# Optimization experiments

Measured on AMD Instinct MI355X. Metric: run time of the kernel, lower is better.

Reference implementation:

```python
import jax, jax.numpy as jnp
import numpy as np

S = 3072      # total tokens across all images
DIM = 1280    # hidden_size
H = 16        # num_heads
HD = DIM // H # head_dim = 80
NSEG = 6      # number of images (cu_seqlens has NSEG+1 entries)


def _rotate_half(x):
    x1, x2 = jnp.split(x, 2, axis=-1)
    return jnp.concatenate([-x2, x1], axis=-1)


def setup_inputs() -> dict:
    key = jax.random.key(0)
    ks = jax.random.split(key, 12)
    hidden_states = jax.random.normal(ks[0], (S, DIM), jnp.float32)
    # realistic vision rotary embedding: half-dim inv_freq, repeated to head_dim
    inv_freq = 1.0 / (10000.0 ** (jnp.arange(0, HD // 2, dtype=jnp.float32) / (HD // 2)))
    freqs = jnp.arange(S, dtype=jnp.float32)[:, None] * inv_freq[None, :]  # [S, HD/2]
    emb = jnp.concatenate([freqs, freqs], axis=-1)  # [S, HD]
    cos = jnp.cos(emb)
    sin = jnp.sin(emb)
    sc = 0.02
    wq = jax.random.normal(ks[1], (DIM, DIM), jnp.float32) * sc
    bq = jax.random.normal(ks[2], (DIM,), jnp.float32) * sc
    wk = jax.random.normal(ks[3], (DIM, DIM), jnp.float32) * sc
    bk = jax.random.normal(ks[4], (DIM,), jnp.float32) * sc
    wv = jax.random.normal(ks[5], (DIM, DIM), jnp.float32) * sc
    bv = jax.random.normal(ks[6], (DIM,), jnp.float32) * sc
    wo = jax.random.normal(ks[7], (DIM, DIM), jnp.float32) * sc
    bo = jax.random.normal(ks[8], (DIM,), jnp.float32) * sc
    cu_seqlens = (jnp.arange(NSEG + 1, dtype=jnp.int32) * (S // NSEG))  # [0,512,...,3072]
    return dict(hidden_states=hidden_states, cos=cos, sin=sin,
                wq=wq, bq=bq, wk=wk, bk=bk, wv=wv, bv=bv, wo=wo, bo=bo,
                cu_seqlens=cu_seqlens)


def reference(hidden_states, cos, sin, wq, bq, wk, bk, wv, bv, wo, bo, cu_seqlens):
    seq_length = hidden_states.shape[0]
    scaling = HD ** (-0.5)
    # QKV projections (torch Linear: x @ W.T + b)
    q = (hidden_states @ wq.T + bq).reshape(seq_length, H, HD)
    k = (hidden_states @ wk.T + bk).reshape(seq_length, H, HD)
    v = (hidden_states @ wv.T + bv).reshape(seq_length, H, HD)
    # apply_rotary_pos_emb_vision: cos/sin [S, HD] broadcast over head axis
    c = cos[:, None, :]
    s = sin[:, None, :]
    q = q * c + _rotate_half(q) * s
    k = k * c + _rotate_half(k) * s
    # block-diagonal (per-image) attention via segment mask
    seg = jnp.searchsorted(cu_seqlens[1:], jnp.arange(seq_length), side='right')
    mask = seg[:, None] == seg[None, :]  # [S, S] bool
    scores = jnp.einsum('shd,thd->hst', q, k) * scaling  # [H, S, S]
    scores = jnp.where(mask[None, :, :], scores, jnp.finfo(scores.dtype).min)
    attn = jax.nn.softmax(scores, axis=-1)
    out = jnp.einsum('hst,thd->shd', attn, v).reshape(seq_length, DIM)
    return out @ wo.T + bo
```

## Files before the change

### kernel.cpp

```cpp
#include <hip/hip_runtime.h>
#include <hip/hip_bf16.h>
#include <hip/hip_fp16.h>
#include <cstdint>
#include <cstddef>

typedef _Float16 f16;
typedef f16 f16x2 __attribute__((ext_vector_type(2)));
typedef f16 f16x4 __attribute__((ext_vector_type(4)));
typedef f16 f16x8 __attribute__((ext_vector_type(8)));
typedef float f32x4 __attribute__((ext_vector_type(4)));

#define S_LEN 3072
#define DIM 1280
#define NH 16
#define HD 80
#define SEG 512

#define MFMA16F(a, b, c) __builtin_amdgcn_mfma_f32_16x16x32_f16((a), (b), (c), 0, 0, 0)

__device__ __forceinline__ void gl2lds16(const void* g, void* l) {
    __builtin_amdgcn_global_load_lds(
        (const __attribute__((address_space(1))) unsigned int*)g,
        (__attribute__((address_space(3))) unsigned int*)l, 16, 0, 0);
}

__device__ __forceinline__ unsigned int pack2(float a, float b) {
    f16x2 t = {(f16)a, (f16)b};
    union { f16x2 v; unsigned int u; } c;
    c.v = t;
    return c.u;
}

__global__ __launch_bounds__(256) void cvt_kernel(
    const float* __restrict__ hs,
    const float* __restrict__ wq, const float* __restrict__ wk,
    const float* __restrict__ wv, const float* __restrict__ wo,
    f16* __restrict__ hs16,
    f16* __restrict__ wq16, f16* __restrict__ wk16,
    f16* __restrict__ wv16, f16* __restrict__ wo16)
{
    const int m = blockIdx.y;
    const float* src; f16* dst; int n4;
    if (m == 0)      { src = hs; dst = hs16; n4 = S_LEN * DIM / 4; }
    else if (m == 1) { src = wq; dst = wq16; n4 = DIM * DIM / 4; }
    else if (m == 2) { src = wk; dst = wk16; n4 = DIM * DIM / 4; }
    else if (m == 3) { src = wv; dst = wv16; n4 = DIM * DIM / 4; }
    else             { src = wo; dst = wo16; n4 = DIM * DIM / 4; }
    int idx = blockIdx.x * 256 + threadIdx.x;
    if (idx >= n4) return;
    f32x4 v = *(const f32x4*)(src + (size_t)idx * 4);
    f16x4 o;
#pragma unroll
    for (int e = 0; e < 4; ++e) o[e] = (f16)v[e];
    *(f16x4*)(dst + (size_t)idx * 4) = o;
}

__global__ __launch_bounds__(256) void gemm_f16_kernel(
    const f16* __restrict__ A,
    const f16* __restrict__ W0, const f16* __restrict__ W1, const f16* __restrict__ W2,
    const float* __restrict__ b0, const float* __restrict__ b1, const float* __restrict__ b2,
    f16* __restrict__ O0, f16* __restrict__ O1, f16* __restrict__ vT)
{
    const int f = blockIdx.x;
    const int xcd = f & 7;
    const int idx = f >> 3;
    const int mt = xcd * 3 + idx % 3;
    const int yz = idx / 3;
    const int nt = yz % 10;
    const int mode = yz / 10;

    const f16* W = (mode == 1) ? W1 : (mode == 2) ? W2 : W0;
    const float* bias = (mode == 1) ? b1 : (mode == 2) ? b2 : b0;

    __shared__ __align__(16) f16 As[128 * 32];
    __shared__ __align__(16) f16 Bs[128 * 32];

    const int tid = threadIdx.x;
    const int lane = tid & 63;
    const int lane15 = tid & 15;
    const int quad = lane >> 4;
    const int w = tid >> 6;
    const int wm = (w >> 1) * 64;
    const int wn = (w & 1) * 64;
    const int m0 = mt * 128;
    const int n0 = nt * 128;

    const int srow = w * 32 + (lane >> 2);
    const int scol = (lane & 3) * 8;
    const f16* gA0 = A + (size_t)(m0 + srow) * DIM + scol;
    const f16* gA1 = A + (size_t)(m0 + srow + 16) * DIM + scol;
    const f16* gB0 = W + (size_t)(n0 + srow) * DIM + scol;
    const f16* gB1 = W + (size_t)(n0 + srow + 16) * DIM + scol;
    f16* lA0 = As + (w * 32) * 32;
    f16* lA1 = As + (w * 32 + 16) * 32;
    f16* lB0 = Bs + (w * 32) * 32;
    f16* lB1 = Bs + (w * 32 + 16) * 32;

    f32x4 acc[4][4];
#pragma unroll
    for (int i = 0; i < 4; ++i)
#pragma unroll
        for (int j = 0; j < 4; ++j)
            acc[i][j] = (f32x4){0.f, 0.f, 0.f, 0.f};

    for (int kt = 0; kt < DIM / 32; ++kt) {
        __syncthreads();
        gl2lds16(gA0 + kt * 32, lA0);
        gl2lds16(gA1 + kt * 32, lA1);
        gl2lds16(gB0 + kt * 32, lB0);
        gl2lds16(gB1 + kt * 32, lB1);
        __syncthreads();

        f16x8 fa[4], fb[4];
#pragma unroll
        for (int i = 0; i < 4; ++i)
            fa[i] = *(const f16x8*)(As + (wm + i * 16 + lane15) * 32 + quad * 8);
#pragma unroll
        for (int j = 0; j < 4; ++j)
            fb[j] = *(const f16x8*)(Bs + (wn + j * 16 + lane15) * 32 + quad * 8);
#pragma unroll
        for (int i = 0; i < 4; ++i)
#pragma unroll
            for (int j = 0; j < 4; ++j)
                acc[i][j] = MFMA16F(fa[i], fb[j], acc[i][j]);
    }

    float bvv[4];
#pragma unroll
    for (int j = 0; j < 4; ++j)
        bvv[j] = bias[n0 + wn + j * 16 + lane15];

    if (mode == 2) {
#pragma unroll
        for (int i = 0; i < 4; ++i)
#pragma unroll
            for (int j = 0; j < 4; ++j) {
                f16x4 ov;
#pragma unroll
                for (int r = 0; r < 4; ++r) ov[r] = (f16)(acc[i][j][r] + bvv[j]);
                int row = m0 + wm + i * 16 + quad * 4;
                int col = n0 + wn + j * 16 + lane15;
                *(f16x4*)(vT + (size_t)col * S_LEN + row) = ov;
            }
    } else {
        f16* O = (mode == 0) ? O0 : O1;
#pragma unroll
        for (int i = 0; i < 4; ++i)
#pragma unroll
            for (int j = 0; j < 4; ++j)
#pragma unroll
                for (int r = 0; r < 4; ++r) {
                    int row = m0 + wm + i * 16 + quad * 4 + r;
                    int col = n0 + wn + j * 16 + lane15;
                    O[(size_t)row * DIM + col] = (f16)(acc[i][j][r] + bvv[j]);
                }
    }
}

__global__ __launch_bounds__(256) void gemm_out_kernel(
    const f16* __restrict__ A, const f16* __restrict__ W,
    const float* __restrict__ bias, float* __restrict__ OF)
{
    const int f = blockIdx.x;
    const int xcd = f & 7;
    const int idx = f >> 3;
    const int xt = xcd * 6 + idx % 6;
    const int yt = idx / 6;

    __shared__ __align__(16) f16 As[64 * 32];
    __shared__ __align__(16) f16 Bs[128 * 32];

    const int tid = threadIdx.x;
    const int lane = tid & 63;
    const int lane15 = tid & 15;
    const int quad = lane >> 4;
    const int w = tid >> 6;
    const int wn = w * 32;
    const int m0 = xt * 64;
    const int n0 = yt * 128;

    const int srA = w * 16 + (lane >> 2);
    const int srB = w * 32 + (lane >> 2);
    const int scol = (lane & 3) * 8;
    const f16* gA0 = A + (size_t)(m0 + srA) * DIM + scol;
    const f16* gB0 = W + (size_t)(n0 + srB) * DIM + scol;
    const f16* gB1 = W + (size_t)(n0 + srB + 16) * DIM + scol;
    f16* lA0 = As + (w * 16) * 32;
    f16* lB0 = Bs + (w * 32) * 32;
    f16* lB1 = Bs + (w * 32 + 16) * 32;

    f32x4 acc[4][2];
#pragma unroll
    for (int i = 0; i < 4; ++i)
#pragma unroll
        for (int j = 0; j < 2; ++j)
            acc[i][j] = (f32x4){0.f, 0.f, 0.f, 0.f};

    for (int kt = 0; kt < DIM / 32; ++kt) {
        __syncthreads();
        gl2lds16(gA0 + kt * 32, lA0);
        gl2lds16(gB0 + kt * 32, lB0);
        gl2lds16(gB1 + kt * 32, lB1);
        __syncthreads();

        f16x8 fa[4], fb[2];
#pragma unroll
        for (int i = 0; i < 4; ++i)
            fa[i] = *(const f16x8*)(As + (i * 16 + lane15) * 32 + quad * 8);
#pragma unroll
        for (int j = 0; j < 2; ++j)
            fb[j] = *(const f16x8*)(Bs + (wn + j * 16 + lane15) * 32 + quad * 8);
#pragma unroll
        for (int i = 0; i < 4; ++i)
#pragma unroll
            for (int j = 0; j < 2; ++j)
                acc[i][j] = MFMA16F(fa[i], fb[j], acc[i][j]);
    }

    float bvv[2];
#pragma unroll
    for (int j = 0; j < 2; ++j)
        bvv[j] = bias[n0 + wn + j * 16 + lane15];

#pragma unroll
    for (int i = 0; i < 4; ++i)
#pragma unroll
        for (int j = 0; j < 2; ++j)
#pragma unroll
            for (int r = 0; r < 4; ++r) {
                int row = m0 + i * 16 + quad * 4 + r;
                int col = n0 + wn + j * 16 + lane15;
                OF[(size_t)row * DIM + col] = acc[i][j][r] + bvv[j];
            }
}

__global__ __launch_bounds__(256) void rope_kernel(
    f16* __restrict__ qb, f16* __restrict__ kb,
    const float* __restrict__ cosb, const float* __restrict__ sinb)
{
    int idx = blockIdx.x * 256 + threadIdx.x;
    int c = idx % 5;
    int t = idx / 5;
    int h = t & 15; t >>= 4;
    int s = t % S_LEN;
    int which = t / S_LEN;
    f16* buf = which ? kb : qb;
    float scale = which ? 1.0f : 0.11180339887498948f;
    int j = c * 8;
    f32x4 ca = *(const f32x4*)(cosb + s * HD + j);
    f32x4 cb = *(const f32x4*)(cosb + s * HD + j + 4);
    f32x4 sna = *(const f32x4*)(sinb + s * HD + j);
    f32x4 snb = *(const f32x4*)(sinb + s * HD + j + 4);
    size_t base = (size_t)s * DIM + h * HD + j;
    f16x8 x1 = *(f16x8*)(buf + base);
    f16x8 x2 = *(f16x8*)(buf + base + 40);
    f16x8 o1, o2;
#pragma unroll
    for (int e = 0; e < 8; ++e) {
        float ce = (e < 4) ? ca[e] : cb[e - 4];
        float se = (e < 4) ? sna[e] : snb[e - 4];
        float a = (float)x1[e], b = (float)x2[e];
        o1[e] = (f16)((a * ce - b * se) * scale);
        o2[e] = (f16)((b * ce + a * se) * scale);
    }
    *(f16x8*)(buf + base) = o1;
    *(f16x8*)(buf + base + 40) = o2;
}

__global__ __launch_bounds__(256) void attn_kernel(
    const f16* __restrict__ q, const f16* __restrict__ k,
    const f16* __restrict__ vT, f16* __restrict__ o)
{
    const int h = blockIdx.x;
    const int g = blockIdx.y;
    const int qc = blockIdx.z;
    const int tid = threadIdx.x;
    const int lane15 = tid & 15;
    const int quad = (tid & 63) >> 4;
    const int w = tid >> 6;
    const int qbase = g * SEG + qc * 64;
    const int qrow = qbase + w * 16 + lane15;

    __shared__ __align__(16) f16 Ks[128 * 88];
    __shared__ __align__(16) f16 Vt[80 * 128];

    f16x8 zf;
#pragma unroll
    for (int e = 0; e < 8; ++e) zf[e] = (f16)0.0f;

    f16x8 fq[3];
#pragma unroll
    for (int kc = 0; kc < 3; ++kc) {
        if (kc == 2 && quad >= 2) fq[kc] = zf;
        else fq[kc] = *(const f16x8*)(q + (size_t)qrow * DIM + h * HD + kc * 32 + quad * 8);
    }

    float m_run = -1e30f, l_run = 0.f;
    f32x4 Oa[5];
#pragma unroll
    for (int dt = 0; dt < 5; ++dt) Oa[dt] = (f32x4){0.f, 0.f, 0.f, 0.f};

    for (int kt = 0; kt < 4; ++kt) {
        __syncthreads();
        const int kb = g * SEG + kt * 128;
#pragma unroll
        for (int c = tid; c < 1280; c += 256) {
            int r = c / 10;
            int c8 = (c - r * 10) * 8;
            *(f16x8*)(Ks + r * 88 + c8) =
                *(const f16x8*)(k + (size_t)(kb + r) * DIM + h * HD + c8);
        }
#pragma unroll
        for (int c = tid; c < 1280; c += 256) {
            int d = c >> 4;
            int sc = c & 15;
            *(f16x8*)(Vt + d * 128 + (sc ^ (d & 7)) * 8) =
                *(const f16x8*)(vT + (size_t)(h * HD + d) * S_LEN + kb + sc * 8);
        }
        __syncthreads();

        f32x4 sa[8];
#pragma unroll
        for (int nt = 0; nt < 8; ++nt) sa[nt] = (f32x4){0.f, 0.f, 0.f, 0.f};
#pragma unroll
        for (int kc = 0; kc < 3; ++kc) {
#pragma unroll
            for (int nt = 0; nt < 8; ++nt) {
                f16x8 fk;
                if (kc == 2 && quad >= 2) fk = zf;
                else fk = *(const f16x8*)(Ks + (nt * 16 + lane15) * 88 + kc * 32 + quad * 8);
                sa[nt] = MFMA16F(fk, fq[kc], sa[nt]);
            }
        }

        float mt = -1e30f;
#pragma unroll
        for (int nt = 0; nt < 8; ++nt)
#pragma unroll
            for (int r = 0; r < 4; ++r) mt = fmaxf(mt, sa[nt][r]);
        mt = fmaxf(mt, __shfl_xor(mt, 16, 64));
        mt = fmaxf(mt, __shfl_xor(mt, 32, 64));

        float mn = fmaxf(m_run, mt);
        float alpha = __expf(m_run - mn);
        m_run = mn;
        float lt = 0.f;
        unsigned int pp[8][2];
#pragma unroll
        for (int nt = 0; nt < 8; ++nt) {
            float p0 = __expf(sa[nt][0] - mn);
            float p1 = __expf(sa[nt][1] - mn);
            float p2 = __expf(sa[nt][2] - mn);
            float p3 = __expf(sa[nt][3] - mn);
            lt += (p0 + p1) + (p2 + p3);
            pp[nt][0] = pack2(p0, p1);
            pp[nt][1] = pack2(p2, p3);
        }
        lt += __shfl_xor(lt, 16, 64);
        lt += __shfl_xor(lt, 32, 64);
        l_run = l_run * alpha + lt;

#pragma unroll
        for (int dt = 0; dt < 5; ++dt)
#pragma unroll
            for (int r = 0; r < 4; ++r) Oa[dt][r] *= alpha;

        const int srcA = ((quad & 1) * 2) * 16 + lane15;
        const int srcB = srcA + 16;
        const bool hi = quad >= 2;
#pragma unroll
        for (int kc2 = 0; kc2 < 4; ++kc2) {
            unsigned int e0 = __shfl((int)pp[2 * kc2][0], srcA, 64);
            unsigned int e1 = __shfl((int)pp[2 * kc2][1], srcA, 64);
            unsigned int e2 = __shfl((int)pp[2 * kc2][0], srcB, 64);
            unsigned int e3 = __shfl((int)pp[2 * kc2][1], srcB, 64);
            unsigned int o0 = __shfl((int)pp[2 * kc2 + 1][0], srcA, 64);
            unsigned int o1 = __shfl((int)pp[2 * kc2 + 1][1], srcA, 64);
            unsigned int o2 = __shfl((int)pp[2 * kc2 + 1][0], srcB, 64);
            unsigned int o3 = __shfl((int)pp[2 * kc2 + 1][1], srcB, 64);
            union { unsigned int u[4]; f16x8 v; } fp;
            fp.u[0] = hi ? o0 : e0;
            fp.u[1] = hi ? o1 : e1;
            fp.u[2] = hi ? o2 : e2;
            fp.u[3] = hi ? o3 : e3;
#pragma unroll
            for (int dt = 0; dt < 5; ++dt) {
                int drow = dt * 16 + lane15;
                int slot = (kc2 * 4 + quad) ^ (drow & 7);
                f16x8 fv = *(const f16x8*)(Vt + drow * 128 + slot * 8);
                Oa[dt] = MFMA16F(fv, fp.v, Oa[dt]);
            }
        }
    }

    float inv = 1.0f / l_run;
#pragma unroll
    for (int dt = 0; dt < 5; ++dt) {
        f16x4 ov;
#pragma unroll
        for (int r = 0; r < 4; ++r) ov[r] = (f16)(Oa[dt][r] * inv);
        *(f16x4*)(o + (size_t)qrow * DIM + h * HD + dt * 16 + quad * 4) = ov;
    }
}

extern "C" void kernel_launch(void* const* d_in, const int* in_sizes, int n_in,
                              void* d_out, int out_size, void* d_ws, size_t ws_size,
                              hipStream_t stream)
{
    const float* hs   = (const float*)d_in[0];
    const float* cosb = (const float*)d_in[1];
    const float* sinb = (const float*)d_in[2];
    const float* wq   = (const float*)d_in[3];
    const float* bq   = (const float*)d_in[4];
    const float* wk   = (const float*)d_in[5];
    const float* bk   = (const float*)d_in[6];
    const float* wv   = (const float*)d_in[7];
    const float* bv   = (const float*)d_in[8];
    const float* wo   = (const float*)d_in[9];
    const float* bo   = (const float*)d_in[10];

    const size_t SD = (size_t)S_LEN * DIM;
    const size_t WW = (size_t)DIM * DIM;
    f16* hs16 = (f16*)d_ws;
    f16* wq16 = hs16 + SD;
    f16* wk16 = wq16 + WW;
    f16* wv16 = wk16 + WW;
    f16* wo16 = wv16 + WW;
    f16* q16  = wo16 + WW;
    f16* k16  = q16 + SD;
    f16* vT16 = k16 + SD;
    f16* ao16 = vT16 + SD;
    float* outb = (float*)d_out;

    cvt_kernel<<<dim3(S_LEN * DIM / 4 / 256, 5), 256, 0, stream>>>(
        hs, wq, wk, wv, wo, hs16, wq16, wk16, wv16, wo16);
    gemm_f16_kernel<<<720, 256, 0, stream>>>(
        hs16, wq16, wk16, wv16, bq, bk, bv, q16, k16, vT16);
    rope_kernel<<<1920, 256, 0, stream>>>(q16, k16, cosb, sinb);
    attn_kernel<<<dim3(NH, 6, 8), 256, 0, stream>>>(q16, k16, vT16, ao16);
    gemm_out_kernel<<<480, 256, 0, stream>>>(ao16, wo16, bo, outb);
}
```

Before: 217.9 us.

## Rewrite QKV GEMM with 256x256 tiles, double-buffered LDS and swizzled layout

Replaces the 128x128 QKV projection kernel with a 256x256-tile, 512-thread kernel that treats the wq/wk/wv f16 copies as one contiguous 3840-row weight matrix. It double-buffers the K=64 slabs in LDS, prefetching the next slab during compute, and uses an XOR-swizzled LDS layout to avoid bank conflicts. MFMA phases are interleaved with barriers and s_setprio. The larger tiles raise data reuse and cut launch count from 720 to 180 blocks, but this may leave CUs underfilled on a 256-CU part and needs 128KB of LDS per block. It also assumes the three weight buffers sit contiguously in the workspace, which they do.

```diff
diff --git a/kernel.cpp b/kernel.cpp
--- a/kernel.cpp
+++ b/kernel.cpp
@@ -55,105 +55,173 @@
     *(f16x4*)(dst + (size_t)idx * 4) = o;
 }
 
-__global__ __launch_bounds__(256) void gemm_f16_kernel(
-    const f16* __restrict__ A,
-    const f16* __restrict__ W0, const f16* __restrict__ W1, const f16* __restrict__ W2,
-    const float* __restrict__ b0, const float* __restrict__ b1, const float* __restrict__ b2,
-    f16* __restrict__ O0, f16* __restrict__ O1, f16* __restrict__ vT)
+__global__ __launch_bounds__(512, 2) void gemm_qkv256(
+    const f16* __restrict__ A, const f16* __restrict__ Wb,
+    const float* __restrict__ bq, const float* __restrict__ bk,
+    const float* __restrict__ bv,
+    f16* __restrict__ q16, f16* __restrict__ k16, f16* __restrict__ vT)
 {
-    const int f = blockIdx.x;
-    const int xcd = f & 7;
-    const int idx = f >> 3;
-    const int mt = xcd * 3 + idx % 3;
-    const int yz = idx / 3;
-    const int nt = yz % 10;
-    const int mode = yz / 10;
-
-    const f16* W = (mode == 1) ? W1 : (mode == 2) ? W2 : W0;
-    const float* bias = (mode == 1) ? b1 : (mode == 2) ? b2 : b0;
-
-    __shared__ __align__(16) f16 As[128 * 32];
-    __shared__ __align__(16) f16 Bs[128 * 32];
+    const int bid = blockIdx.x;
+    const int mt = bid / 15;
+    const int nt = bid % 15;
+    const int m0 = mt * 256;
+    const int n0 = nt * 256;
+
+    __shared__ __align__(16) f16 Abuf[2][256 * 64];
+    __shared__ __align__(16) f16 Bbuf[2][256 * 64];
 
     const int tid = threadIdx.x;
+    const int w = tid >> 6;
     const int lane = tid & 63;
-    const int lane15 = tid & 15;
+    const int lane15 = lane & 15;
     const int quad = lane >> 4;
-    const int w = tid >> 6;
-    const int wm = (w >> 1) * 64;
-    const int wn = (w & 1) * 64;
-    const int m0 = mt * 128;
-    const int n0 = nt * 128;
-
-    const int srow = w * 32 + (lane >> 2);
-    const int scol = (lane & 3) * 8;
-    const f16* gA0 = A + (size_t)(m0 + srow) * DIM + scol;
-    const f16* gA1 = A + (size_t)(m0 + srow + 16) * DIM + scol;
-    const f16* gB0 = W + (size_t)(n0 + srow) * DIM + scol;
-    const f16* gB1 = W + (size_t)(n0 + srow + 16) * DIM + scol;
-    f16* lA0 = As + (w * 32) * 32;
-    f16* lA1 = As + (w * 32 + 16) * 32;
-    f16* lB0 = Bs + (w * 32) * 32;
-    f16* lB1 = Bs + (w * 32 + 16) * 32;
-
-    f32x4 acc[4][4];
-#pragma unroll
-    for (int i = 0; i < 4; ++i)
+    const int wm = (w >> 2) * 128;
+    const int wn = (w & 3) * 64;
+
+    const int srow = lane >> 3;
+    const int schk = (lane & 7) ^ srow;
+    const f16* gA = A  + (size_t)(m0 + w * 32 + srow) * DIM + schk * 8;
+    const f16* gB = Wb + (size_t)(n0 + w * 32 + srow) * DIM + schk * 8;
+
+    const int x7 = lane15 & 7;
+    const int cc0 = (quad ^ x7) * 8;
+    const int cc1 = ((quad + 4) ^ x7) * 8;
+
+    f32x4 acc[8][4];
+#pragma unroll
+    for (int i = 0; i < 8; ++i)
 #pragma unroll
         for (int j = 0; j < 4; ++j)
             acc[i][j] = (f32x4){0.f, 0.f, 0.f, 0.f};
 
-    for (int kt = 0; kt < DIM / 32; ++kt) {
-        __syncthreads();
-        gl2lds16(gA0 + kt * 32, lA0);
-        gl2lds16(gA1 + kt * 32, lA1);
-        gl2lds16(gB0 + kt * 32, lB0);
-        gl2lds16(gB1 + kt * 32, lB1);
-        __syncthreads();
-
-        f16x8 fa[4], fb[4];
+#pragma unroll
+    for (int c = 0; c < 4; ++c)
+        gl2lds16(gA + (size_t)c * 8 * DIM, Abuf[0] + (w * 4 + c) * 512);
+#pragma unroll
+    for (int c = 0; c < 4; ++c)
+        gl2lds16(gB + (size_t)c * 8 * DIM, Bbuf[0] + (w * 4 + c) * 512);
+    asm volatile("s_waitcnt vmcnt(0)" ::: "memory");
+    __builtin_amdgcn_s_barrier();
+
+    for (int kt = 0; kt < 20; ++kt) {
+        const int s = kt & 1;
+        const f16* As = Abuf[s];
+        const f16* Bs = Bbuf[s];
+
+        if (kt < 19) {
+            const f16* gA1 = gA + (kt + 1) * 64;
+            const f16* gB1 = gB + (kt + 1) * 64;
+            f16* lA = Abuf[s ^ 1] + w * 4 * 512;
+            f16* lB = Bbuf[s ^ 1] + w * 4 * 512;
+#pragma unroll
+            for (int c = 0; c < 4; ++c) gl2lds16(gA1 + (size_t)c * 8 * DIM, lA + c * 512);
+#pragma unroll
+            for (int c = 0; c < 4; ++c) gl2lds16(gB1 + (size_t)c * 8 * DIM, lB + c * 512);
+        }
+        f16x8 a0[4][2], b01[2][2];
+#pragma unroll
+        for (int i = 0; i < 4; ++i) {
+            const f16* rp = As + (wm + i * 16 + lane15) * 64;
+            a0[i][0] = *(const f16x8*)(rp + cc0);
+            a0[i][1] = *(const f16x8*)(rp + cc1);
+        }
+#pragma unroll
+        for (int j = 0; j < 2; ++j) {
+            const f16* rp = Bs + (wn + j * 16 + lane15) * 64;
+            b01[j][0] = *(const f16x8*)(rp + cc0);
+            b01[j][1] = *(const f16x8*)(rp + cc1);
+        }
+        __builtin_amdgcn_s_setprio(1);
 #pragma unroll
         for (int i = 0; i < 4; ++i)
-            fa[i] = *(const f16x8*)(As + (wm + i * 16 + lane15) * 32 + quad * 8);
-#pragma unroll
-        for (int j = 0; j < 4; ++j)
-            fb[j] = *(const f16x8*)(Bs + (wn + j * 16 + lane15) * 32 + quad * 8);
+#pragma unroll
+            for (int j = 0; j < 2; ++j) {
+                acc[i][j] = MFMA16F(a0[i][0], b01[j][0], acc[i][j]);
+                acc[i][j] = MFMA16F(a0[i][1], b01[j][1], acc[i][j]);
+            }
+        __builtin_amdgcn_s_setprio(0);
+        __builtin_amdgcn_s_barrier();
+
+        f16x8 b23[2][2];
+#pragma unroll
+        for (int j = 0; j < 2; ++j) {
+            const f16* rp = Bs + (wn + (j + 2) * 16 + lane15) * 64;
+            b23[j][0] = *(const f16x8*)(rp + cc0);
+            b23[j][1] = *(const f16x8*)(rp + cc1);
+        }
+        __builtin_amdgcn_s_setprio(1);
 #pragma unroll
         for (int i = 0; i < 4; ++i)
 #pragma unroll
+            for (int j = 0; j < 2; ++j) {
+                acc[i][j + 2] = MFMA16F(a0[i][0], b23[j][0], acc[i][j + 2]);
+                acc[i][j + 2] = MFMA16F(a0[i][1], b23[j][1], acc[i][j + 2]);
+            }
+        __builtin_amdgcn_s_setprio(0);
+        __builtin_amdgcn_s_barrier();
+
+        f16x8 a1[4][2];
+#pragma unroll
+        for (int i = 0; i < 4; ++i) {
+            const f16* rp = As + (wm + (i + 4) * 16 + lane15) * 64;
+            a1[i][0] = *(const f16x8*)(rp + cc0);
+            a1[i][1] = *(const f16x8*)(rp + cc1);
+        }
+        __builtin_amdgcn_s_setprio(1);
+#pragma unroll
+        for (int i = 0; i < 4; ++i)
+#pragma unroll
+            for (int j = 0; j < 2; ++j) {
+                acc[i + 4][j + 2] = MFMA16F(a1[i][0], b23[j][0], acc[i + 4][j + 2]);
+                acc[i + 4][j + 2] = MFMA16F(a1[i][1], b23[j][1], acc[i + 4][j + 2]);
+            }
+        __builtin_amdgcn_s_setprio(0);
+        __builtin_amdgcn_s_barrier();
+
+        __builtin_amdgcn_s_setprio(1);
+#pragma unroll
+        for (int i = 0; i < 4; ++i)
+#pragma unroll
+            for (int j = 0; j < 2; ++j) {
+                acc[i + 4][j] = MFMA16F(a1[i][0], b01[j][0], acc[i + 4][j]);
+                acc[i + 4][j] = MFMA16F(a1[i][1], b01[j][1], acc[i + 4][j]);
+            }
+        __builtin_amdgcn_s_setprio(0);
+        asm volatile("s_waitcnt vmcnt(0)" ::: "memory");
+        __builtin_amdgcn_s_barrier();
+    }
+
+    const int sel = nt / 5;
+    const int nc0 = n0 - sel * 1280 + wn;
+    const float* bias = (sel == 0) ? bq : (sel == 1) ? bk : bv;
+    float bvv[4];
+#pragma unroll
+    for (int j = 0; j < 4; ++j) bvv[j] = bias[nc0 + j * 16 + lane15];
+
+    if (sel < 2) {
+        f16* O = sel ? k16 : q16;
+#pragma unroll
+        for (int i = 0; i < 8; ++i)
+#pragma unroll
             for (int j = 0; j < 4; ++j)
-                acc[i][j] = MFMA16F(fa[i], fb[j], acc[i][j]);
-    }
-
-    float bvv[4];
-#pragma unroll
-    for (int j = 0; j < 4; ++j)
-        bvv[j] = bias[n0 + wn + j * 16 + lane15];
-
-    if (mode == 2) {
-#pragma unroll
-        for (int i = 0; i < 4; ++i)
+#pragma unroll
+                for (int r = 0; r < 4; ++r) {
+                    int row = m0 + wm + i * 16 + quad * 4 + r;
+                    O[(size_t)row * DIM + nc0 + j * 16 + lane15] =
+                        (f16)(acc[i][j][r] + bvv[j]);
+                }
+    } else {
+#pragma unroll
+        for (int i = 0; i < 8; ++i)
 #pragma unroll
             for (int j = 0; j < 4; ++j) {
                 f16x4 ov;
 #pragma unroll
                 for (int r = 0; r < 4; ++r) ov[r] = (f16)(acc[i][j][r] + bvv[j]);
                 int row = m0 + wm + i * 16 + quad * 4;
-                int col = n0 + wn + j * 16 + lane15;
+                int col = nc0 + j * 16 + lane15;
                 *(f16x4*)(vT + (size_t)col * S_LEN + row) = ov;
             }
-    } else {
-        f16* O = (mode == 0) ? O0 : O1;
-#pragma unroll
-        for (int i = 0; i < 4; ++i)
-#pragma unroll
-            for (int j = 0; j < 4; ++j)
-#pragma unroll
-                for (int r = 0; r < 4; ++r) {
-                    int row = m0 + wm + i * 16 + quad * 4 + r;
-                    int col = n0 + wn + j * 16 + lane15;
-                    O[(size_t)row * DIM + col] = (f16)(acc[i][j][r] + bvv[j]);
-                }
     }
 }
 
@@ -434,8 +502,8 @@
 
     cvt_kernel<<<dim3(S_LEN * DIM / 4 / 256, 5), 256, 0, stream>>>(
         hs, wq, wk, wv, wo, hs16, wq16, wk16, wv16, wo16);
-    gemm_f16_kernel<<<720, 256, 0, stream>>>(
-        hs16, wq16, wk16, wv16, bq, bk, bv, q16, k16, vT16);
+    gemm_qkv256<<<180, 512, 0, stream>>>(
+        hs16, wq16, bq, bk, bv, q16, k16, vT16);
     rope_kernel<<<1920, 256, 0, stream>>>(q16, k16, cosb, sinb);
     attn_kernel<<<dim3(NH, 6, 8), 256, 0, stream>>>(q16, k16, vT16, ao16);
     gemm_out_kernel<<<480, 256, 0, stream>>>(ao16, wo16, bo, outb);
```

New measurement: 231.0 us. +6.0%, slower.
